# Optimization experiments

Measured on AMD Instinct MI355X. Metric: run time of the kernel, lower is better.

Reference implementation:

```python
import jax, jax.numpy as jnp
import numpy as np
from jax import lax

# 4D spatial convolution dimension numbers: batch, channel, 4 spatial axes (X,Y,Z,W)
DN = ('NCXYZW', 'OIXYZW', 'NCXYZW')


def setup_inputs() -> dict:
    key = jax.random.key(0)
    k1, k2, k3, k4, k5 = jax.random.split(key, 5)
    B, S, K = 512, 18, 13
    x = jax.random.normal(k1, (B, 1, S, S, S, S), dtype=jnp.float32)
    # conv4d(1, 3, 13): weight [out=3, in=1, 13,13,13,13], torch-style init scale
    fan_in = 1 * K ** 4
    conv_w = jax.random.normal(k2, (3, 1, K, K, K, K), dtype=jnp.float32) / np.sqrt(fan_in)
    conv_b = jax.random.normal(k3, (3,), dtype=jnp.float32) * 0.01
    # Linear(3 * 6**4 = 3888, 1)
    lin_w = jax.random.normal(k4, (1, 3888), dtype=jnp.float32) / np.sqrt(3888)
    lin_b = jax.random.normal(k5, (1,), dtype=jnp.float32) * 0.01
    return {'x': x, 'conv_w': conv_w, 'conv_b': conv_b, 'lin_w': lin_w, 'lin_b': lin_b}


def reference(x, conv_w, conv_b, lin_w, lin_b):
    # 4D conv (cross-correlation, matching torch), VALID padding, stride 1
    h = lax.conv_general_dilated(
        x, conv_w,
        window_strides=(1, 1, 1, 1),
        padding='VALID',
        dimension_numbers=DN,
    )  # [B, 3, 6, 6, 6, 6]
    h = h + conv_b[None, :, None, None, None, None]
    h = jax.nn.relu(h)
    # Flatten (channel-major, same as torch.flatten) -> [B, 3888]
    h = h.reshape(h.shape[0], -1)
    # Dropout(0.5) is identity in eval mode. Linear + Sigmoid.
    logits = h @ lin_w.T + lin_b  # [B, 1]
    return jax.nn.sigmoid(logits)
```

## Files before the change

kernel.cpp:

```cpp
#include <hip/hip_runtime.h>

typedef unsigned short u16;
typedef __bf16 v8bf __attribute__((ext_vector_type(8)));
typedef float v4f __attribute__((ext_vector_type(4)));
typedef u16 v8u16 __attribute__((ext_vector_type(8)));

#define X_B 104976
#define X_A 5832
#define X_P 324
#define XB_B 106272
#define XB_A 5904
#define XB_P 328
#define XB_ELEMS 54411328u
#define KP 59488
#define SLAB 352
#define NPAD 112
#define B2_ELEMS 6662656u
#define C_ELEMS 2064384u
#define KSPLIT 7
#define NBLK (72 * KSPLIT)
#define MT_FAST 74
#define NBLK_FAST (74 * 13)
#define WS_C   0
#define WS_B2  8257536ull
#define WS_XB  21582848ull
#define WS_FAST_NEED 130405504ull

__device__ __forceinline__ u16 f2bf(float f) {
    unsigned u = __builtin_bit_cast(unsigned, f);
    u += 0x7fffu + ((u >> 16) & 1u);
    return (u16)(u >> 16);
}

#define AS1C(p) (const __attribute__((address_space(1))) void*)(p)
#define AS3(p)  (__attribute__((address_space(3))) void*)(p)
#define WAIT_VM3 0x0F73
#define WAIT_VM2 0x0F72
#define WAIT_VM1 0x0F71
#define WAIT_VM0 0x0F70

__global__ void conv_bf16_kernel(const float* __restrict__ X, u16* __restrict__ Xb) {
    const int bx = blockIdx.x;
    if (bx == 0 && threadIdx.x < 64) Xb[54411264u + threadIdx.x] = 0;
    const long xbbase = (long)bx * XB_A;
    const long xfbase = (long)bx * X_A;
    for (int s = threadIdx.x; s < 738; s += 256) {
        int y = s / 41;
        int pos = (s - y * 41) * 8;
        const float* src = X + xfbase + y * 324 + pos;
        float4 lo = *(const float4*)src;
        float4 hi = (pos + 4 < 324) ? *(const float4*)(src + 4)
                                    : make_float4(0.f, 0.f, 0.f, 0.f);
        v8u16 p;
        p[0] = f2bf(lo.x); p[1] = f2bf(lo.y); p[2] = f2bf(lo.z); p[3] = f2bf(lo.w);
        p[4] = f2bf(hi.x); p[5] = f2bf(hi.y); p[6] = f2bf(hi.z); p[7] = f2bf(hi.w);
        *(v8u16*)(Xb + xbbase + s * 8) = p;
    }
}

template<bool B3MODE>
__global__ void build_b2_kernel(const float* __restrict__ W, u16* __restrict__ B2,
                                float* __restrict__ C) {
    unsigned t = blockIdx.x * 256u + threadIdx.x;
    if (t < 516096u) ((float4*)C)[t] = make_float4(0.f, 0.f, 0.f, 0.f);
    if (t >= 832832u) return;
    unsigned n, slab, jj0;
    if (B3MODE) {
        unsigned kx = t / 64064u;
        unsigned r = t - kx * 64064u;
        unsigned g = r / 448u;
        unsigned bslot = r - g * 448u;
        n = bslot >> 2;
        unsigned chunk = (bslot & 3u) ^ ((bslot >> 3) & 3u);
        unsigned si = g / 13u, kyq = g - si * 13u;
        slab = kx * 13u + kyq;
        jj0 = si * 32u + chunk * 8u;
    } else {
        n = t / 7436u;
        unsigned k0 = (t - n * 7436u) * 8u;
        slab = k0 / 352u;
        jj0 = k0 - slab * 352u;
    }
    v8u16 out = {0, 0, 0, 0, 0, 0, 0, 0};
    if (n < 108u && jj0 < 324u) {
        unsigned kx = slab / 13u, ky = slab - kx * 13u;
        unsigned o = n / 36u, zw = n - o * 36u;
        unsigned zo = zw / 6u, wo = zw - zo * 6u;
        const float* wb = W + o * 28561u + kx * 2197u + ky * 169u;
#pragma unroll
        for (int e = 0; e < 8; ++e) {
            unsigned jj = jj0 + e;
            if (jj < 324u) {
                unsigned jz = jj / 18u, jw = jj - jz * 18u;
                int dz = (int)jz - (int)zo, dw = (int)jw - (int)wo;
                if (dz >= 0 && dz < 13 && dw >= 0 && dw < 13)
                    out[e] = f2bf(wb[dz * 13 + dw]);
            }
        }
    }
    ((v8u16*)B2)[t] = out;
}

__global__ __launch_bounds__(512, 4) void gemm_conv_fast(
    const u16* __restrict__ Xb, const u16* __restrict__ B3, float* __restrict__ C)
{
    __shared__ u16 Alds[3072 * 8];
    __shared__ u16 Blds[4][112 * 32];

    const int tid = threadIdx.x;
    const int lane = tid & 63;
    const int wv = tid >> 6;
    const int bwv = (wv < 7) ? wv : 6;
    const int mt = blockIdx.x % MT_FAST;
    const int kx = blockIdx.x / MT_FAST;
    const int b0 = mt * 7;

    const int bslot = bwv * 64 + lane;
    const u16* laneBp = B3 + ((kx * 143) * 448 + bslot) * 8;

    int fr_base[2], fr_p0[2];
#pragma unroll
    for (int i = 0; i < 2; ++i) {
        int row = wv * 32 + i * 16 + (lane & 15);
        if (row > 251) row = 251;
        int bl = row / 36, xy = row - bl * 36;
        int x = xy / 6, y = xy - x * 6;
        fr_p0[i] = x * 18 + y;
        fr_base[i] = bl * 432;
    }
    const int fc = lane >> 4;

    auto stageA = [&](int si_, int j) {
        int q = j * 512 + tid;
        int qe = (q >= 3024) ? q - 3024 : q;
        int bl = qe / 432;
        int rem = qe - bl * 432;
        int p = rem >> 2;
        int pos = rem & 3;
        int c = pos ^ ((p >> 1) & 3);
        int b = b0 + bl; if (b > 511) b = 511;
        int prow = p / 18;
        int pcol = p - prow * 18;
        const u16* gp = Xb + (b * XB_B + (kx + prow) * XB_A + pcol * XB_P
                              + si_ * 32 + c * 8);
        __builtin_amdgcn_global_load_lds(AS1C(gp),
            AS3(&Alds[(j * 512 + wv * 64) * 8]), 16, 0, 0);
    };
    auto stageB = [&](int g_, int pb_) {
        const u16* gp = laneBp + g_ * 3584;
        __builtin_amdgcn_global_load_lds(AS1C(gp),
            AS3(&Blds[pb_][(bwv * 64) * 8]), 16, 0, 0);
    };

    v4f acc[2][7];
#pragma unroll
    for (int i = 0; i < 2; ++i)
#pragma unroll
        for (int t = 0; t < 7; ++t) acc[i][t] = (v4f){0.f, 0.f, 0.f, 0.f};

#pragma unroll
    for (int j = 0; j < 6; ++j) stageA(0, j);
    stageB(0, 0);
    stageB(1, 1);
    stageB(2, 2);

    int si = 0, ky = 0;

    for (int g = 0; g < 143; ++g) {
        if (ky == 0 && si > 0) {
            __builtin_amdgcn_s_barrier();
#pragma unroll
            for (int j = 0; j < 6; ++j) stageA(si, j);
            stageB(g + 3, (g + 3) & 3);
            __builtin_amdgcn_s_waitcnt(WAIT_VM1);
            __builtin_amdgcn_s_barrier();
        } else {
            int rem = 142 - g;
            if (rem >= 2)      __builtin_amdgcn_s_waitcnt(WAIT_VM2);
            else if (rem == 1) __builtin_amdgcn_s_waitcnt(WAIT_VM1);
            else               __builtin_amdgcn_s_waitcnt(WAIT_VM0);
            __builtin_amdgcn_s_barrier();
            if (g + 3 < 143) stageB(g + 3, (g + 3) & 3);
        }

        v8bf a[2];
#pragma unroll
        for (int i = 0; i < 2; ++i) {
            int p = fr_p0[i] + ky;
            int slot = fr_base[i] + p * 4 + (fc ^ ((p >> 1) & 3));
            a[i] = *(const v8bf*)(&Alds[slot * 8]);
        }
        const int pb = g & 3;
#pragma unroll
        for (int t = 0; t < 7; ++t) {
            int row = t * 16 + (lane & 15);
            int slot = row * 4 + ((lane >> 4) ^ ((row >> 1) & 3));
            v8bf bb = *(const v8bf*)(&Blds[pb][slot * 8]);
#pragma unroll
            for (int i = 0; i < 2; ++i)
                acc[i][t] = __builtin_amdgcn_mfma_f32_16x16x32_bf16(a[i], bb, acc[i][t], 0, 0, 0);
        }

        if (++ky == 13) { ky = 0; ++si; }
    }

    const int colb = lane & 15;
    const int rq = (lane >> 4) * 4;
#pragma unroll
    for (int i = 0; i < 2; ++i) {
        int rl0 = wv * 32 + i * 16 + rq;
#pragma unroll
        for (int t = 0; t < 7; ++t) {
            int col = t * 16 + colb;
#pragma unroll
            for (int gq = 0; gq < 4; ++gq) {
                int lr = rl0 + gq;
                int grow = mt * 252 + lr;
                if (lr < 252 && grow < 18432)
                    atomicAdd(&C[grow * NPAD + col], acc[i][t][gq]);
            }
        }
    }
}

template<bool USE_XB>
__global__ __launch_bounds__(512, 4) void gemm_conv(
    const u16* __restrict__ Xb, const float* __restrict__ Xf,
    const u16* __restrict__ B2, float* __restrict__ C)
{
    __shared__ u16 Alds[3][256 * 32];
    __shared__ u16 Blds[3][112 * 32];

    const int tid = threadIdx.x;
    const int lane = tid & 63;
    const int wv = tid >> 6;
    const int bwv = (wv < 7) ? wv : 6;
    const int mt = blockIdx.x % 72;
    const int ks = blockIdx.x / 72;

    const int sbeg = (ks * 169) / KSPLIT;
    const int send = ((ks + 1) * 169) / KSPLIT;
    const int nsteps = (send - sbeg) * 11;

    int laneA[2], chunkA[2];
#pragma unroll
    for (int jr = 0; jr < 2; ++jr) {
        int slot = jr * 512 + tid;
        int row = slot >> 2;
        int chunk = (slot & 3) ^ ((slot >> 3) & 3);
        int r = mt * 256 + row;
        int b = r / 36;
        int xy = r - b * 36;
        int x = xy / 6;
        int y = xy - x * 6;
        if (USE_XB) laneA[jr] = b * XB_B + x * XB_A + y * XB_P + chunk * 8;
        else        laneA[jr] = b * X_B + x * X_A + y * X_P;
        chunkA[jr] = chunk;
    }
    const int bslot = bwv * 64 + lane;
    const int chunkB = (bslot & 3) ^ ((bslot >> 3) & 3);
    const int laneB = (bslot >> 2) * KP + chunkB * 8;

    v4f acc[2][7];
#pragma unroll
    for (int i = 0; i < 2; ++i)
#pragma unroll
        for (int t = 0; t < 7; ++t) acc[i][t] = (v4f){0.f, 0.f, 0.f, 0.f};

    auto stage = [&](int step, int p) {
        int q = step / 11;
        int si = step - q * 11;
        int slab = sbeg + q;
        int kx = slab / 13;
        int ky = slab - kx * 13;
        if (USE_XB) {
            int aofs = kx * XB_A + ky * XB_P + si * 32;
#pragma unroll
            for (int jr = 0; jr < 2; ++jr) {
                const u16* gp = Xb + (laneA[jr] + aofs);
                __builtin_amdgcn_global_load_lds(AS1C(gp), AS3(&Alds[p][(jr * 512 + wv * 64) * 8]), 16, 0, 0);
            }
        } else {
            int aofs = kx * X_A + ky * X_P;
#pragma unroll
            for (int jr = 0; jr < 2; ++jr) {
                int jj0 = si * 32 + chunkA[jr] * 8;
                const float* gp = Xf + (laneA[jr] + aofs);
                float4 lo = make_float4(0.f, 0.f, 0.f, 0.f);
                float4 hi = make_float4(0.f, 0.f, 0.f, 0.f);
                if (jj0 < 324)     lo = *(const float4*)(gp + jj0);
                if (jj0 + 4 < 324) hi = *(const float4*)(gp + jj0 + 4);
                v8u16 pk;
                pk[0] = f2bf(lo.x); pk[1] = f2bf(lo.y); pk[2] = f2bf(lo.z); pk[3] = f2bf(lo.w);
                pk[4] = f2bf(hi.x); pk[5] = f2bf(hi.y); pk[6] = f2bf(hi.z); pk[7] = f2bf(hi.w);
                int slot = jr * 512 + tid;
                *(v8u16*)(&Alds[p][slot * 8]) = pk;
            }
        }
        int bofs = slab * SLAB + si * 32;
        const u16* gp0 = B2 + (laneB + bofs);
        __builtin_amdgcn_global_load_lds(AS1C(gp0), AS3(&Blds[p][(bwv * 64) * 8]), 16, 0, 0);
    };

    stage(0, 0);
    stage(1, 1);

    for (int step = 0; step < nsteps; ++step) {
        const int p = step % 3;
        if (USE_XB) {
            if (step + 1 < nsteps) __builtin_amdgcn_s_waitcnt(WAIT_VM3);
            else                   __builtin_amdgcn_s_waitcnt(WAIT_VM0);
        } else {
            __builtin_amdgcn_s_waitcnt(0);
        }
        __builtin_amdgcn_s_barrier();
        if (step + 2 < nsteps) stage(step + 2, (step + 2) % 3);

        v8bf a[2];
#pragma unroll
        for (int i = 0; i < 2; ++i) {
            int row = wv * 32 + i * 16 + (lane & 15);
            int slot = row * 4 + ((lane >> 4) ^ ((row >> 1) & 3));
            a[i] = *(const v8bf*)(&Alds[p][slot * 8]);
        }
#pragma unroll
        for (int t = 0; t < 7; ++t) {
            int row = t * 16 + (lane & 15);
            int slot = row * 4 + ((lane >> 4) ^ ((row >> 1) & 3));
            v8bf bb = *(const v8bf*)(&Blds[p][slot * 8]);
#pragma unroll
            for (int i = 0; i < 2; ++i)
                acc[i][t] = __builtin_amdgcn_mfma_f32_16x16x32_bf16(a[i], bb, acc[i][t], 0, 0, 0);
        }
    }

    const int colb = lane & 15;
    const int rq = (lane >> 4) * 4;
#pragma unroll
    for (int i = 0; i < 2; ++i) {
        int rowb = mt * 256 + wv * 32 + i * 16 + rq;
#pragma unroll
        for (int t = 0; t < 7; ++t) {
            int col = t * 16 + colb;
#pragma unroll
            for (int g = 0; g < 4; ++g)
                atomicAdd(&C[(rowb + g) * NPAD + col], acc[i][t][g]);
        }
    }
}

__global__ void epilogue_kernel(const float* __restrict__ C, const float* __restrict__ cb,
                                const float* __restrict__ lw, const float* __restrict__ lb,
                                float* __restrict__ out) {
    const int b = blockIdx.x;
    const int tid = threadIdx.x;
    float s = 0.f;
    for (int t = tid; t < 3888; t += 256) {
        int xy = t / 108, n = t - xy * 108;
        int o = n / 36, zw = n - o * 36;
        int x = xy / 6, y = xy - x * 6;
        float c = C[(b * 36 + xy) * NPAD + n] + cb[o];
        s += fmaxf(c, 0.f) * lw[o * 1296 + x * 216 + y * 36 + zw];
    }
#pragma unroll
    for (int off = 32; off > 0; off >>= 1) s += __shfl_down(s, off, 64);
    __shared__ float red[4];
    if ((tid & 63) == 0) red[tid >> 6] = s;
    __syncthreads();
    if (tid == 0)
        out[b] = 1.f / (1.f + expf(-(red[0] + red[1] + red[2] + red[3] + lb[0])));
}

extern "C" void kernel_launch(void* const* d_in, const int* in_sizes, int n_in,
                              void* d_out, int out_size, void* d_ws, size_t ws_size,
                              hipStream_t stream) {
    const float* X  = (const float*)d_in[0];
    const float* W  = (const float*)d_in[1];
    const float* cb = (const float*)d_in[2];
    const float* lw = (const float*)d_in[3];
    const float* lb = (const float*)d_in[4];
    float* out = (float*)d_out;
    char* ws = (char*)d_ws;
    float* C  = (float*)(ws + WS_C);
    u16* B2   = (u16*)(ws + WS_B2);
    u16* Xb   = (u16*)(ws + WS_XB);
    const bool fast = ws_size >= WS_FAST_NEED;

    if (fast) {
        build_b2_kernel<true><<<3254, 256, 0, stream>>>(W, B2, C);
        conv_bf16_kernel<<<9216, 256, 0, stream>>>(X, Xb);
        gemm_conv_fast<<<NBLK_FAST, 512, 0, stream>>>(Xb, B2, C);
    } else {
        build_b2_kernel<false><<<3254, 256, 0, stream>>>(W, B2, C);
        gemm_conv<false><<<NBLK, 512, 0, stream>>>(nullptr, X, B2, C);
    }
    epilogue_kernel<<<512, 256, 0, stream>>>(C, cb, lw, lb, out);
}
```

Baseline: 688.6 us.

## Load B fragments directly from global into registers and fuse prep kernels

The fast GEMM no longer stages the B3 weight tiles through LDS with a 4-deep buffer and per-step barriers. Each lane now reads its B fragments straight from global memory into registers, prefetching the next step's fragments while issuing the current MFMAs, so barriers are needed only when the A tile is restaged. The bf16 conversion of X and the B3/C initialisation are merged into one prep launch to save a kernel launch. The cost is more register pressure, and global-load latency is exposed whenever one step's MFMAs cannot hide it.

```diff
diff --git a/kernel.cpp b/kernel.cpp
--- a/kernel.cpp
+++ b/kernel.cpp
@@ -11,12 +11,10 @@
 #define XB_B 106272
 #define XB_A 5904
 #define XB_P 328
-#define XB_ELEMS 54411328u
 #define KP 59488
 #define SLAB 352
 #define NPAD 112
 #define B2_ELEMS 6662656u
-#define C_ELEMS 2064384u
 #define KSPLIT 7
 #define NBLK (72 * KSPLIT)
 #define MT_FAST 74
@@ -35,88 +33,77 @@
 #define AS1C(p) (const __attribute__((address_space(1))) void*)(p)
 #define AS3(p)  (__attribute__((address_space(3))) void*)(p)
 #define WAIT_VM3 0x0F73
-#define WAIT_VM2 0x0F72
-#define WAIT_VM1 0x0F71
 #define WAIT_VM0 0x0F70
 
-__global__ void conv_bf16_kernel(const float* __restrict__ X, u16* __restrict__ Xb) {
+__global__ void prep_kernel(const float* __restrict__ X, u16* __restrict__ Xb,
+                            const float* __restrict__ W, u16* __restrict__ B3,
+                            float* __restrict__ C) {
     const int bx = blockIdx.x;
-    if (bx == 0 && threadIdx.x < 64) Xb[54411264u + threadIdx.x] = 0;
-    const long xbbase = (long)bx * XB_A;
-    const long xfbase = (long)bx * X_A;
-    for (int s = threadIdx.x; s < 738; s += 256) {
-        int y = s / 41;
-        int pos = (s - y * 41) * 8;
-        const float* src = X + xfbase + y * 324 + pos;
-        float4 lo = *(const float4*)src;
-        float4 hi = (pos + 4 < 324) ? *(const float4*)(src + 4)
-                                    : make_float4(0.f, 0.f, 0.f, 0.f);
-        v8u16 p;
-        p[0] = f2bf(lo.x); p[1] = f2bf(lo.y); p[2] = f2bf(lo.z); p[3] = f2bf(lo.w);
-        p[4] = f2bf(hi.x); p[5] = f2bf(hi.y); p[6] = f2bf(hi.z); p[7] = f2bf(hi.w);
-        *(v8u16*)(Xb + xbbase + s * 8) = p;
-    }
-}
-
-template<bool B3MODE>
-__global__ void build_b2_kernel(const float* __restrict__ W, u16* __restrict__ B2,
-                                float* __restrict__ C) {
-    unsigned t = blockIdx.x * 256u + threadIdx.x;
-    if (t < 516096u) ((float4*)C)[t] = make_float4(0.f, 0.f, 0.f, 0.f);
-    if (t >= 832832u) return;
-    unsigned n, slab, jj0;
-    if (B3MODE) {
+    if (bx < 9216) {
+        if (bx == 0 && threadIdx.x < 64) Xb[54411264u + threadIdx.x] = 0;
+        const long xbbase = (long)bx * XB_A;
+        const long xfbase = (long)bx * X_A;
+        for (int s = threadIdx.x; s < 738; s += 256) {
+            int y = s / 41;
+            int pos = (s - y * 41) * 8;
+            const float* src = X + xfbase + y * 324 + pos;
+            float4 lo = *(const float4*)src;
+            float4 hi = (pos + 4 < 324) ? *(const float4*)(src + 4)
+                                        : make_float4(0.f, 0.f, 0.f, 0.f);
+            v8u16 p;
+            p[0] = f2bf(lo.x); p[1] = f2bf(lo.y); p[2] = f2bf(lo.z); p[3] = f2bf(lo.w);
+            p[4] = f2bf(hi.x); p[5] = f2bf(hi.y); p[6] = f2bf(hi.z); p[7] = f2bf(hi.w);
+            *(v8u16*)(Xb + xbbase + s * 8) = p;
+        }
+    } else {
+        unsigned t = (unsigned)(bx - 9216) * 256u + threadIdx.x;
+        if (t < 516096u) ((float4*)C)[t] = make_float4(0.f, 0.f, 0.f, 0.f);
+        if (t >= 832832u) return;
         unsigned kx = t / 64064u;
         unsigned r = t - kx * 64064u;
         unsigned g = r / 448u;
         unsigned bslot = r - g * 448u;
-        n = bslot >> 2;
+        unsigned n = bslot >> 2;
         unsigned chunk = (bslot & 3u) ^ ((bslot >> 3) & 3u);
         unsigned si = g / 13u, kyq = g - si * 13u;
-        slab = kx * 13u + kyq;
-        jj0 = si * 32u + chunk * 8u;
-    } else {
-        n = t / 7436u;
-        unsigned k0 = (t - n * 7436u) * 8u;
-        slab = k0 / 352u;
-        jj0 = k0 - slab * 352u;
-    }
-    v8u16 out = {0, 0, 0, 0, 0, 0, 0, 0};
-    if (n < 108u && jj0 < 324u) {
-        unsigned kx = slab / 13u, ky = slab - kx * 13u;
-        unsigned o = n / 36u, zw = n - o * 36u;
-        unsigned zo = zw / 6u, wo = zw - zo * 6u;
-        const float* wb = W + o * 28561u + kx * 2197u + ky * 169u;
-#pragma unroll
-        for (int e = 0; e < 8; ++e) {
-            unsigned jj = jj0 + e;
-            if (jj < 324u) {
-                unsigned jz = jj / 18u, jw = jj - jz * 18u;
-                int dz = (int)jz - (int)zo, dw = (int)jw - (int)wo;
-                if (dz >= 0 && dz < 13 && dw >= 0 && dw < 13)
-                    out[e] = f2bf(wb[dz * 13 + dw]);
-            }
-        }
-    }
-    ((v8u16*)B2)[t] = out;
+        unsigned slab = kx * 13u + kyq;
+        unsigned jj0 = si * 32u + chunk * 8u;
+        v8u16 out = {0, 0, 0, 0, 0, 0, 0, 0};
+        if (n < 108u && jj0 < 324u) {
+            unsigned o = n / 36u, zw = n - o * 36u;
+            unsigned zo = zw / 6u, wo = zw - zo * 6u;
+            unsigned ky = slab - kx * 13u;
+            const float* wb = W + o * 28561u + kx * 2197u + ky * 169u;
+#pragma unroll
+            for (int e = 0; e < 8; ++e) {
+                unsigned jj = jj0 + e;
+                if (jj < 324u) {
+                    unsigned jz = jj / 18u, jw = jj - jz * 18u;
+                    int dz = (int)jz - (int)zo, dw = (int)jw - (int)wo;
+                    if (dz >= 0 && dz < 13 && dw >= 0 && dw < 13)
+                        out[e] = f2bf(wb[dz * 13 + dw]);
+                }
+            }
+        }
+        ((v8u16*)B3)[t] = out;
+    }
 }
 
 __global__ __launch_bounds__(512, 4) void gemm_conv_fast(
     const u16* __restrict__ Xb, const u16* __restrict__ B3, float* __restrict__ C)
 {
     __shared__ u16 Alds[3072 * 8];
-    __shared__ u16 Blds[4][112 * 32];
 
     const int tid = threadIdx.x;
     const int lane = tid & 63;
     const int wv = tid >> 6;
-    const int bwv = (wv < 7) ? wv : 6;
     const int mt = blockIdx.x % MT_FAST;
     const int kx = blockIdx.x / MT_FAST;
     const int b0 = mt * 7;
-
-    const int bslot = bwv * 64 + lane;
-    const u16* laneBp = B3 + ((kx * 143) * 448 + bslot) * 8;
+    const int fc = lane >> 4;
+
+    const u16* bptr = B3 + (size_t)kx * 512512u
+                    + ((lane & 15) * 4 + (fc ^ (((lane & 15) >> 1) & 3))) * 8;
 
     int fr_base[2], fr_p0[2];
 #pragma unroll
@@ -128,7 +115,6 @@
         fr_p0[i] = x * 18 + y;
         fr_base[i] = bl * 432;
     }
-    const int fc = lane >> 4;
 
     auto stageA = [&](int si_, int j) {
         int q = j * 512 + tid;
@@ -146,11 +132,6 @@
         __builtin_amdgcn_global_load_lds(AS1C(gp),
             AS3(&Alds[(j * 512 + wv * 64) * 8]), 16, 0, 0);
     };
-    auto stageB = [&](int g_, int pb_) {
-        const u16* gp = laneBp + g_ * 3584;
-        __builtin_amdgcn_global_load_lds(AS1C(gp),
-            AS3(&Blds[pb_][(bwv * 64) * 8]), 16, 0, 0);
-    };
 
     v4f acc[2][7];
 #pragma unroll
@@ -160,48 +141,54 @@
 
 #pragma unroll
     for (int j = 0; j < 6; ++j) stageA(0, j);
-    stageB(0, 0);
-    stageB(1, 1);
-    stageB(2, 2);
+    v8bf b[7];
+#pragma unroll
+    for (int t = 0; t < 7; ++t) b[t] = *(const v8bf*)(bptr + t * 512);
+    __builtin_amdgcn_s_waitcnt(WAIT_VM0);
+    __builtin_amdgcn_s_barrier();
 
     int si = 0, ky = 0;
 
     for (int g = 0; g < 143; ++g) {
-        if (ky == 0 && si > 0) {
-            __builtin_amdgcn_s_barrier();
-#pragma unroll
-            for (int j = 0; j < 6; ++j) stageA(si, j);
-            stageB(g + 3, (g + 3) & 3);
-            __builtin_amdgcn_s_waitcnt(WAIT_VM1);
-            __builtin_amdgcn_s_barrier();
+        v8bf a0, a1;
+        {
+            int p = fr_p0[0] + ky;
+            int slot = fr_base[0] + p * 4 + (fc ^ ((p >> 1) & 3));
+            a0 = *(const v8bf*)(&Alds[slot * 8]);
+        }
+        {
+            int p = fr_p0[1] + ky;
+            int slot = fr_base[1] + p * 4 + (fc ^ ((p >> 1) & 3));
+            a1 = *(const v8bf*)(&Alds[slot * 8]);
+        }
+        const u16* bnext = bptr + 3584;
+        if (g < 142) {
+#pragma unroll
+            for (int t = 0; t < 7; ++t) {
+                v8bf bt = b[t];
+                acc[0][t] = __builtin_amdgcn_mfma_f32_16x16x32_bf16(a0, bt, acc[0][t], 0, 0, 0);
+                acc[1][t] = __builtin_amdgcn_mfma_f32_16x16x32_bf16(a1, bt, acc[1][t], 0, 0, 0);
+                b[t] = *(const v8bf*)(bnext + t * 512);
+            }
         } else {
-            int rem = 142 - g;
-            if (rem >= 2)      __builtin_amdgcn_s_waitcnt(WAIT_VM2);
-            else if (rem == 1) __builtin_amdgcn_s_waitcnt(WAIT_VM1);
-            else               __builtin_amdgcn_s_waitcnt(WAIT_VM0);
-            __builtin_amdgcn_s_barrier();
-            if (g + 3 < 143) stageB(g + 3, (g + 3) & 3);
-        }
-
-        v8bf a[2];
-#pragma unroll
-        for (int i = 0; i < 2; ++i) {
-            int p = fr_p0[i] + ky;
-            int slot = fr_base[i] + p * 4 + (fc ^ ((p >> 1) & 3));
-            a[i] = *(const v8bf*)(&Alds[slot * 8]);
-        }
-        const int pb = g & 3;
-#pragma unroll
-        for (int t = 0; t < 7; ++t) {
-            int row = t * 16 + (lane & 15);
-            int slot = row * 4 + ((lane >> 4) ^ ((row >> 1) & 3));
-            v8bf bb = *(const v8bf*)(&Blds[pb][slot * 8]);
-#pragma unroll
-            for (int i = 0; i < 2; ++i)
-                acc[i][t] = __builtin_amdgcn_mfma_f32_16x16x32_bf16(a[i], bb, acc[i][t], 0, 0, 0);
-        }
-
-        if (++ky == 13) { ky = 0; ++si; }
+#pragma unroll
+            for (int t = 0; t < 7; ++t) {
+                acc[0][t] = __builtin_amdgcn_mfma_f32_16x16x32_bf16(a0, b[t], acc[0][t], 0, 0, 0);
+                acc[1][t] = __builtin_amdgcn_mfma_f32_16x16x32_bf16(a1, b[t], acc[1][t], 0, 0, 0);
+            }
+        }
+        bptr = bnext;
+
+        if (++ky == 13) {
+            ky = 0; ++si;
+            if (si < 11) {
+                __builtin_amdgcn_s_barrier();
+#pragma unroll
+                for (int j = 0; j < 6; ++j) stageA(si, j);
+                __builtin_amdgcn_s_waitcnt(WAIT_VM0);
+                __builtin_amdgcn_s_barrier();
+            }
+        }
     }
 
     const int colb = lane & 15;
@@ -223,10 +210,37 @@
     }
 }
 
-template<bool USE_XB>
+__global__ void build_b2_kernel(const float* __restrict__ W, u16* __restrict__ B2,
+                                float* __restrict__ C) {
+    unsigned t = blockIdx.x * 256u + threadIdx.x;
+    if (t < 516096u) ((float4*)C)[t] = make_float4(0.f, 0.f, 0.f, 0.f);
+    if (t >= 832832u) return;
+    unsigned n = t / 7436u;
+    unsigned k0 = (t - n * 7436u) * 8u;
+    unsigned slab = k0 / 352u;
+    unsigned jj0 = k0 - slab * 352u;
+    v8u16 out = {0, 0, 0, 0, 0, 0, 0, 0};
+    if (n < 108u && jj0 < 324u) {
+        unsigned kx = slab / 13u, ky = slab - kx * 13u;
+        unsigned o = n / 36u, zw = n - o * 36u;
+        unsigned zo = zw / 6u, wo = zw - zo * 6u;
+        const float* wb = W + o * 28561u + kx * 2197u + ky * 169u;
+#pragma unroll
+        for (int e = 0; e < 8; ++e) {
+            unsigned jj = jj0 + e;
+            if (jj < 324u) {
+                unsigned jz = jj / 18u, jw = jj - jz * 18u;
+                int dz = (int)jz - (int)zo, dw = (int)jw - (int)wo;
+                if (dz >= 0 && dz < 13 && dw >= 0 && dw < 13)
+                    out[e] = f2bf(wb[dz * 13 + dw]);
+            }
+        }
+    }
+    ((v8u16*)B2)[t] = out;
+}
+
 __global__ __launch_bounds__(512, 4) void gemm_conv(
-    const u16* __restrict__ Xb, const float* __restrict__ Xf,
-    const u16* __restrict__ B2, float* __restrict__ C)
+    const float* __restrict__ Xf, const u16* __restrict__ B2, float* __restrict__ C)
 {
     __shared__ u16 Alds[3][256 * 32];
     __shared__ u16 Blds[3][112 * 32];
@@ -253,8 +267,7 @@
         int xy = r - b * 36;
         int x = xy / 6;
         int y = xy - x * 6;
-        if (USE_XB) laneA[jr] = b * XB_B + x * XB_A + y * XB_P + chunk * 8;
-        else        laneA[jr] = b * X_B + x * X_A + y * X_P;
+        laneA[jr] = b * X_B + x * X_A + y * X_P;
         chunkA[jr] = chunk;
     }
     const int bslot = bwv * 64 + lane;
@@ -273,29 +286,20 @@
         int slab = sbeg + q;
         int kx = slab / 13;
         int ky = slab - kx * 13;
-        if (USE_XB) {
-            int aofs = kx * XB_A + ky * XB_P + si * 32;
-#pragma unroll
-            for (int jr = 0; jr < 2; ++jr) {
-                const u16* gp = Xb + (laneA[jr] + aofs);
-                __builtin_amdgcn_global_load_lds(AS1C(gp), AS3(&Alds[p][(jr * 512 + wv * 64) * 8]), 16, 0, 0);
-            }
-        } else {
-            int aofs = kx * X_A + ky * X_P;
-#pragma unroll
-            for (int jr = 0; jr < 2; ++jr) {
-                int jj0 = si * 32 + chunkA[jr] * 8;
-                const float* gp = Xf + (laneA[jr] + aofs);
-                float4 lo = make_float4(0.f, 0.f, 0.f, 0.f);
-                float4 hi = make_float4(0.f, 0.f, 0.f, 0.f);
-                if (jj0 < 324)     lo = *(const float4*)(gp + jj0);
-                if (jj0 + 4 < 324) hi = *(const float4*)(gp + jj0 + 4);
-                v8u16 pk;
-                pk[0] = f2bf(lo.x); pk[1] = f2bf(lo.y); pk[2] = f2bf(lo.z); pk[3] = f2bf(lo.w);
-                pk[4] = f2bf(hi.x); pk[5] = f2bf(hi.y); pk[6] = f2bf(hi.z); pk[7] = f2bf(hi.w);
-                int slot = jr * 512 + tid;
-                *(v8u16*)(&Alds[p][slot * 8]) = pk;
-            }
+        int aofs = kx * X_A + ky * X_P;
+#pragma unroll
+        for (int jr = 0; jr < 2; ++jr) {
+            int jj0 = si * 32 + chunkA[jr] * 8;
+            const float* gp = Xf + (laneA[jr] + aofs);
+            float4 lo = make_float4(0.f, 0.f, 0.f, 0.f);
+            float4 hi = make_float4(0.f, 0.f, 0.f, 0.f);
+            if (jj0 < 324)     lo = *(const float4*)(gp + jj0);
+            if (jj0 + 4 < 324) hi = *(const float4*)(gp + jj0 + 4);
+            v8u16 pk;
+            pk[0] = f2bf(lo.x); pk[1] = f2bf(lo.y); pk[2] = f2bf(lo.z); pk[3] = f2bf(lo.w);
+            pk[4] = f2bf(hi.x); pk[5] = f2bf(hi.y); pk[6] = f2bf(hi.z); pk[7] = f2bf(hi.w);
+            int slot = jr * 512 + tid;
+            *(v8u16*)(&Alds[p][slot * 8]) = pk;
         }
         int bofs = slab * SLAB + si * 32;
         const u16* gp0 = B2 + (laneB + bofs);
@@ -307,12 +311,7 @@
 
     for (int step = 0; step < nsteps; ++step) {
         const int p = step % 3;
-        if (USE_XB) {
-            if (step + 1 < nsteps) __builtin_amdgcn_s_waitcnt(WAIT_VM3);
-            else                   __builtin_amdgcn_s_waitcnt(WAIT_VM0);
-        } else {
-            __builtin_amdgcn_s_waitcnt(0);
-        }
+        __builtin_amdgcn_s_waitcnt(0);
         __builtin_amdgcn_s_barrier();
         if (step + 2 < nsteps) stage(step + 2, (step + 2) % 3);
 
@@ -387,12 +386,11 @@
     const bool fast = ws_size >= WS_FAST_NEED;
 
     if (fast) {
-        build_b2_kernel<true><<<3254, 256, 0, stream>>>(W, B2, C);
-        conv_bf16_kernel<<<9216, 256, 0, stream>>>(X, Xb);
+        prep_kernel<<<12470, 256, 0, stream>>>(X, Xb, W, B2, C);
         gemm_conv_fast<<<NBLK_FAST, 512, 0, stream>>>(Xb, B2, C);
     } else {
-        build_b2_kernel<false><<<3254, 256, 0, stream>>>(W, B2, C);
-        gemm_conv<false><<<NBLK, 512, 0, stream>>>(nullptr, X, B2, C);
+        build_b2_kernel<<<3254, 256, 0, stream>>>(W, B2, C);
+        gemm_conv<<<NBLK, 512, 0, stream>>>(X, B2, C);
     }
     epilogue_kernel<<<512, 256, 0, stream>>>(C, cb, lw, lb, out);
 }
```

Result: faster. 669.5 us (-2.8%).
